# Performance work log

Measured on AMD Instinct MI355X. Metric: run time of the kernel, lower is better.

Reference implementation:

```python
import jax, jax.numpy as jnp
import numpy as np

K, D, B, T = 512, 256, 32, 4096

def setup_inputs() -> dict:
    key = jax.random.key(0)
    k1, k2 = jax.random.split(key)
    z_e_x = jax.random.normal(k1, (B, D, T), dtype=jnp.float32)
    # nn.Embedding weight init uniform(-1/K, 1/K)
    emb_weight = jax.random.uniform(k2, (K, D), dtype=jnp.float32, minval=-1.0 / K, maxval=1.0 / K)
    return {"z_e_x": z_e_x, "emb_weight": emb_weight}

def reference(z_e_x, emb_weight):
    # forward(): permute [B,D,T] -> [B,T,D], nearest-codebook indices
    z = jnp.transpose(z_e_x, (0, 2, 1))  # [B, T, D]
    # squared L2 distances: ||z||^2 - 2 z.W^T + ||W||^2  -> [B, T, K]
    z_sq = jnp.sum(z * z, axis=-1, keepdims=True)           # [B, T, 1]
    w_sq = jnp.sum(emb_weight * emb_weight, axis=-1)        # [K]
    cross = jnp.einsum('btd,kd->btk', z, emb_weight)        # [B, T, K]
    dists = z_sq - 2.0 * cross + w_sq[None, None, :]
    latents = jnp.argmin(dists, axis=-1)                    # [B, T] int
    return latents
```

## Files before the change

kernel.cpp:

```cpp
#include <hip/hip_runtime.h>
#include <math.h>

#define NK 512
#define DD 256
#define NB 32
#define NT 4096

typedef __attribute__((ext_vector_type(8))) _Float16 f16x8;
typedef __attribute__((ext_vector_type(4))) float f32x4;

#define MARGIN 1.5e-4f
#define DCH 16
#define NCH 16
#define APAD 40

__device__ __forceinline__ unsigned short f16bits(float x) {
    _Float16 h = (_Float16)x;
    unsigned short s;
    __builtin_memcpy(&s, &h, 2);
    return s;
}

__global__ __launch_bounds__(512) void prep_kernel(const float* __restrict__ W,
                                                   unsigned short* __restrict__ Wpp,
                                                   float* __restrict__ wsq,
                                                   int* __restrict__ gcnt) {
    const int bx = blockIdx.x;
    const int k  = threadIdx.x;
    if (bx < NCH) {
        const int d0 = bx * DCH;
        float w[16];
        const float4* src4 = (const float4*)(W + (size_t)k * DD + d0);
        #pragma unroll
        for (int q = 0; q < 4; ++q) {
            float4 v = src4[q];
            w[4 * q + 0] = v.x; w[4 * q + 1] = v.y; w[4 * q + 2] = v.z; w[4 * q + 3] = v.w;
        }
        __align__(16) unsigned int dw[16];
        #pragma unroll
        for (int j = 0; j < 16; ++j) {
            unsigned short s = f16bits(w[j] * 4096.0f);
            dw[j] = (unsigned int)s | ((unsigned int)s << 16);
        }
        unsigned short* dst = Wpp + ((size_t)bx * 512 + k) * 32;
        #pragma unroll
        for (int j = 0; j < 4; ++j) ((int4*)dst)[j] = ((const int4*)dw)[j];
    } else {
        const float4* row = (const float4*)(W + (size_t)k * DD);
        double s = 0.0;
        #pragma unroll 8
        for (int i = 0; i < DD / 4; ++i) {
            float4 v = row[i];
            s += (double)v.x * v.x + (double)v.y * v.y + (double)v.z * v.z + (double)v.w * v.w;
        }
        wsq[k] = (float)s;
        if (k == 0) *gcnt = 0;
    }
}

__global__ __launch_bounds__(512, 2) void vq_phase1(const float* __restrict__ Z,
                                                    const unsigned short* __restrict__ Wpp,
                                                    const float* __restrict__ wsq,
                                                    int* __restrict__ out,
                                                    int* __restrict__ gties,
                                                    int* __restrict__ gcnt) {
    __shared__ __align__(16) short As[2][128 * APAD];
    __shared__ __align__(16) short Bs[2][512 * APAD];
    __shared__ double zred[512];
    __shared__ float  zf[128];
    __shared__ float  cb1[512], cb2[512];
    __shared__ int    cbi[512];
    __shared__ int    llist[128];
    __shared__ int    lcnt, gbase;

    const int tid  = threadIdx.x;
    const int wave = tid >> 6;
    const int lane = tid & 63;
    const int lm   = lane & 15;
    const int lq   = lane >> 4;
    const int mw   = wave & 1;
    const int nw   = wave >> 1;

    const int bx = blockIdx.x;
    const int b  = bx >> 5;
    const int t0 = (bx & 31) * 128;

    const int t_l = tid & 127;
    const int dg  = tid >> 7;

    const float* zcol = Z + (size_t)b * DD * NT + t0 + t_l;
    const unsigned short* wrow = Wpp + (size_t)tid * 32;

    if (tid == 0) lcnt = 0;

    f32x4 acc[4][8];
    #pragma unroll
    for (int mt = 0; mt < 4; ++mt)
        #pragma unroll
        for (int nt = 0; nt < 8; ++nt)
            acc[mt][nt] = (f32x4){0.f, 0.f, 0.f, 0.f};

    double zacc = 0.0;

    {
        float zv[4];
        #pragma unroll
        for (int j = 0; j < 4; ++j)
            zv[j] = zcol[(size_t)(dg * 4 + j) * NT];
        int4 wv[4];
        const int4* ws4 = (const int4*)wrow;
        #pragma unroll
        for (int q = 0; q < 4; ++q) wv[q] = ws4[q];

        #pragma unroll
        for (int j = 0; j < 4; ++j) zacc = fma((double)zv[j], (double)zv[j], zacc);
        __align__(16) unsigned int u[4];
        #pragma unroll
        for (int j = 0; j < 4; ++j) {
            _Float16 zh = (_Float16)zv[j];
            float rz = zv[j] - (float)zh;
            unsigned short hs, ls;
            __builtin_memcpy(&hs, &zh, 2);
            ls = f16bits(rz);
            u[j] = (unsigned int)hs | ((unsigned int)ls << 16);
        }
        *(int4*)&As[0][t_l * APAD + dg * 8] = *(const int4*)u;
        int4* bd = (int4*)&Bs[0][tid * APAD];
        bd[0] = wv[0]; bd[1] = wv[1]; bd[2] = wv[2]; bd[3] = wv[3];
    }
    __syncthreads();

    for (int c = 0; c < NCH; ++c) {
        const int cur = c & 1;

        float zv2[4]; int4 wv2[4];
        if (c < NCH - 1) {
            const int d0 = (c + 1) * DCH;
            #pragma unroll
            for (int j = 0; j < 4; ++j)
                zv2[j] = zcol[(size_t)(d0 + dg * 4 + j) * NT];
            const int4* ws4 = (const int4*)(wrow + (size_t)(c + 1) * NK * 32);
            #pragma unroll
            for (int q = 0; q < 4; ++q) wv2[q] = ws4[q];
        }

        f16x8 a[4], bb[8];
        #pragma unroll
        for (int mt = 0; mt < 4; ++mt)
            a[mt] = *(const f16x8*)&As[cur][(mw * 64 + mt * 16 + lm) * APAD + lq * 8];
        #pragma unroll
        for (int nt = 0; nt < 8; ++nt)
            bb[nt] = *(const f16x8*)&Bs[cur][(nw * 128 + nt * 16 + lm) * APAD + lq * 8];
        #pragma unroll
        for (int mt = 0; mt < 4; ++mt)
            #pragma unroll
            for (int nt = 0; nt < 8; ++nt)
                acc[mt][nt] = __builtin_amdgcn_mfma_f32_16x16x32_f16(
                    a[mt], bb[nt], acc[mt][nt], 0, 0, 0);

        if (c < NCH - 1) {
            #pragma unroll
            for (int j = 0; j < 4; ++j) zacc = fma((double)zv2[j], (double)zv2[j], zacc);
            __align__(16) unsigned int u[4];
            #pragma unroll
            for (int j = 0; j < 4; ++j) {
                _Float16 zh = (_Float16)zv2[j];
                float rz = zv2[j] - (float)zh;
                unsigned short hs, ls;
                __builtin_memcpy(&hs, &zh, 2);
                ls = f16bits(rz);
                u[j] = (unsigned int)hs | ((unsigned int)ls << 16);
            }
            *(int4*)&As[cur ^ 1][t_l * APAD + dg * 8] = *(const int4*)u;
            int4* bd = (int4*)&Bs[cur ^ 1][tid * APAD];
            bd[0] = wv2[0]; bd[1] = wv2[1]; bd[2] = wv2[2]; bd[3] = wv2[3];
            __syncthreads();
        }
    }

    zred[dg * 128 + t_l] = zacc;
    __syncthreads();
    if (tid < 128)
        zf[tid] = (float)(((zred[tid] + zred[128 + tid]) + zred[256 + tid]) + zred[384 + tid]);
    __syncthreads();

    float wq[8];
    #pragma unroll
    for (int nt = 0; nt < 8; ++nt)
        wq[nt] = wsq[nw * 128 + nt * 16 + lm];
    const int kbase = nw * 128 + lm;

    #pragma unroll
    for (int mt = 0; mt < 4; ++mt) {
        #pragma unroll
        for (int r = 0; r < 4; ++r) {
            float zz = zf[mw * 64 + mt * 16 + lq * 4 + r];
            float q1 = INFINITY, q2 = INFINITY;
            int i1 = 0x7fffffff;
            #pragma unroll
            for (int nt = 0; nt < 8; ++nt) {
                float c2   = __fmul_rn(acc[mt][nt][r], 4.8828125e-4f);
                float dist = __fadd_rn(__fsub_rn(zz, c2), wq[nt]);
                int kk = kbase + nt * 16;
                if (dist < q1 || (dist == q1 && kk < i1)) { q2 = q1; q1 = dist; i1 = kk; }
                else if (dist < q2) q2 = dist;
            }
            #pragma unroll
            for (int mk = 1; mk <= 8; mk <<= 1) {
                float o1 = __shfl_xor(q1, mk);
                float o2 = __shfl_xor(q2, mk);
                int   oi = __shfl_xor(i1, mk);
                if (o1 < q1 || (o1 == q1 && oi < i1)) { q2 = fminf(q1, o2); q1 = o1; i1 = oi; }
                else { q2 = fminf(o1, q2); }
            }
            if (lm == 0) {
                int m = mw * 64 + mt * 16 + lq * 4 + r;
                cb1[m * 4 + nw] = q1;
                cb2[m * 4 + nw] = q2;
                cbi[m * 4 + nw] = i1;
            }
        }
    }
    __syncthreads();
    if (tid < 128) {
        float q1 = cb1[tid * 4], q2 = cb2[tid * 4];
        int   i1 = cbi[tid * 4];
        #pragma unroll
        for (int p = 1; p < 4; ++p) {
            float c1 = cb1[tid * 4 + p], c2v = cb2[tid * 4 + p];
            int   ci = cbi[tid * 4 + p];
            if (c1 < q1 || (c1 == q1 && ci < i1)) { q2 = fminf(q1, c2v); q1 = c1; i1 = ci; }
            else { q2 = fminf(q2, c1); }
        }
        out[(size_t)b * NT + t0 + tid] = i1;
        if (q2 - q1 <= MARGIN) {
            int p = atomicAdd(&lcnt, 1);
            llist[p] = b * NT + t0 + tid;
        }
    }
    __syncthreads();
    if (tid == 0) gbase = (lcnt > 0) ? atomicAdd(gcnt, lcnt) : 0;
    __syncthreads();
    if (tid < lcnt) gties[gbase + tid] = llist[tid];
}

__global__ __launch_bounds__(256) void vq_fix(const float* __restrict__ Z,
                                              const float* __restrict__ W,
                                              const float* __restrict__ wsq,
                                              const int* __restrict__ gties,
                                              const int* __restrict__ gcnt,
                                              int* __restrict__ out) {
    __shared__ __align__(16) float Zs[8][256];
    __shared__ double pz[8][32];
    __shared__ float  zsqs[8];
    __shared__ int    bts[8];
    __shared__ float  rv[8][4];
    __shared__ int    ri[8][4];

    const int tid  = threadIdx.x;
    const int lane = tid & 63;
    const int wvx  = tid >> 6;
    const int n    = *gcnt;

    for (int base = blockIdx.x * 8; base < n; base += (int)gridDim.x * 8) {
        const int m = (n - base < 8) ? (n - base) : 8;
        __syncthreads();
        if (tid < 8) bts[tid] = gties[base + ((tid < m) ? tid : 0)];
        __syncthreads();

        #pragma unroll
        for (int i = 0; i < 8; ++i) {
            if (i < m) {
                int tb = bts[i];
                int bb = tb >> 12, t = tb & 4095;
                Zs[i][tid] = Z[(size_t)bb * DD * NT + (size_t)tid * NT + t];
            }
        }
        __syncthreads();

        {
            int i = tid >> 5, seg = tid & 31;
            double s = 0.0;
            #pragma unroll
            for (int j = 0; j < 8; ++j) {
                double zz = (double)Zs[i][seg * 8 + j];
                s = fma(zz, zz, s);
            }
            pz[i][seg] = s;
        }
        __syncthreads();
        if (tid < 8) {
            double s = 0.0;
            #pragma unroll
            for (int j = 0; j < 32; ++j) s += pz[tid][j];
            zsqs[tid] = (float)s;
        }
        __syncthreads();

        float da[2][8];
        #pragma unroll
        for (int rr = 0; rr < 2; ++rr) {
            int k = tid + rr * 256;
            const float4* wr = (const float4*)(W + (size_t)k * DD);
            float a8[8];
            #pragma unroll
            for (int i = 0; i < 8; ++i) a8[i] = 0.f;
            #pragma unroll 2
            for (int q = 0; q < 64; ++q) {
                float4 w4 = wr[q];
                #pragma unroll
                for (int i = 0; i < 8; ++i) {
                    float4 z4 = *(const float4*)&Zs[i][4 * q];
                    a8[i] = fmaf(z4.x, w4.x, a8[i]);
                    a8[i] = fmaf(z4.y, w4.y, a8[i]);
                    a8[i] = fmaf(z4.z, w4.z, a8[i]);
                    a8[i] = fmaf(z4.w, w4.w, a8[i]);
                }
            }
            float wqv = wsq[k];
            #pragma unroll
            for (int i = 0; i < 8; ++i)
                da[rr][i] = __fadd_rn(__fsub_rn(zsqs[i], __fmul_rn(2.0f, a8[i])), wqv);
        }

        #pragma unroll
        for (int i = 0; i < 8; ++i) {
            float v = da[0][i]; int ix = tid;
            if (da[1][i] < v) { v = da[1][i]; ix = tid + 256; }
            #pragma unroll
            for (int mk = 1; mk <= 32; mk <<= 1) {
                float ov = __shfl_xor(v, mk);
                int   oi = __shfl_xor(ix, mk);
                if (ov < v || (ov == v && oi < ix)) { v = ov; ix = oi; }
            }
            if (lane == 0) { rv[i][wvx] = v; ri[i][wvx] = ix; }
        }
        __syncthreads();
        if (tid < 8 && tid < m) {
            float v = INFINITY; int ix = 0x7fffffff;
            #pragma unroll
            for (int w = 0; w < 4; ++w) {
                if (rv[tid][w] < v || (rv[tid][w] == v && ri[tid][w] < ix)) {
                    v = rv[tid][w]; ix = ri[tid][w];
                }
            }
            out[bts[tid]] = ix;
        }
    }
}

#define BT 128
#define BK 128
#define DCHUNK 32
#define NKC (NK / BK)
#define NDC (DD / DCHUNK)
#define WSTR (BK + 4)

__global__ __launch_bounds__(256) void vq_fallback(const float* __restrict__ Z,
                                                   const float* __restrict__ W,
                                                   int* __restrict__ out) {
    __shared__ __align__(16) float Zs[DCHUNK * BT];
    __shared__ __align__(16) float Ws[DCHUNK * WSTR];
    __shared__ float wsqs[NK];

    const int tid = threadIdx.x;
    const int tx  = tid & 15;
    const int ty  = tid >> 4;
    const int b   = blockIdx.y;
    const int t0  = blockIdx.x * BT;

    for (int k = tid; k < NK; k += 256) {
        const float4* row = (const float4*)(W + (size_t)k * DD);
        double s = 0.0;
        for (int i = 0; i < DD / 4; ++i) {
            float4 v = row[i];
            s += (double)v.x * v.x + (double)v.y * v.y + (double)v.z * v.z + (double)v.w * v.w;
        }
        wsqs[k] = (float)s;
    }

    const float* Zb = Z + (size_t)b * DD * NT + t0;

    float best[8]; int bidx[8];
    #pragma unroll
    for (int a = 0; a < 8; ++a) { best[a] = INFINITY; bidx[a] = 0x7fffffff; }
    double zsqd[8];
    #pragma unroll
    for (int a = 0; a < 8; ++a) zsqd[a] = 0.0;
    float zsqf[8];

    for (int kc = 0; kc < NKC; ++kc) {
        float acc[8][8];
        #pragma unroll
        for (int a = 0; a < 8; ++a)
            #pragma unroll
            for (int c = 0; c < 8; ++c) acc[a][c] = 0.f;

        for (int dc = 0; dc < NDC; ++dc) {
            const int d0 = dc * DCHUNK;
            __syncthreads();
            #pragma unroll
            for (int i = 0; i < 4; ++i) {
                int f  = tid + i * 256;
                int r  = f >> 5;
                int c4 = f & 31;
                float4 v = *(const float4*)(Zb + (size_t)(d0 + r) * NT + c4 * 4);
                *(float4*)(&Zs[r * BT + c4 * 4]) = v;
            }
            #pragma unroll
            for (int i = 0; i < 4; ++i) {
                int u  = tid + i * 256;
                int k  = u >> 3;
                int rg = u & 7;
                float4 v = *(const float4*)(W + (size_t)(kc * BK + k) * DD + d0 + rg * 4);
                Ws[(rg * 4 + 0) * WSTR + k] = v.x;
                Ws[(rg * 4 + 1) * WSTR + k] = v.y;
                Ws[(rg * 4 + 2) * WSTR + k] = v.z;
                Ws[(rg * 4 + 3) * WSTR + k] = v.w;
            }
            __syncthreads();
            #pragma unroll 4
            for (int d = 0; d < DCHUNK; ++d) {
                float4 z0 = *(const float4*)(&Zs[d * BT + ty * 8]);
                float4 z1 = *(const float4*)(&Zs[d * BT + ty * 8 + 4]);
                float4 w0 = *(const float4*)(&Ws[d * WSTR + tx * 8]);
                float4 w1 = *(const float4*)(&Ws[d * WSTR + tx * 8 + 4]);
                float za[8] = {z0.x, z0.y, z0.z, z0.w, z1.x, z1.y, z1.z, z1.w};
                float wa[8] = {w0.x, w0.y, w0.z, w0.w, w1.x, w1.y, w1.z, w1.w};
                if (kc == 0) {
                    #pragma unroll
                    for (int a = 0; a < 8; ++a)
                        zsqd[a] = fma((double)za[a], (double)za[a], zsqd[a]);
                }
                #pragma unroll
                for (int a = 0; a < 8; ++a)
                    #pragma unroll
                    for (int c = 0; c < 8; ++c)
                        acc[a][c] = fmaf(za[a], wa[c], acc[a][c]);
            }
        }
        if (kc == 0) {
            #pragma unroll
            for (int a = 0; a < 8; ++a) zsqf[a] = (float)zsqd[a];
        }
        #pragma unroll
        for (int c = 0; c < 8; ++c) {
            int   kg = kc * BK + tx * 8 + c;
            float wqv = wsqs[kg];
            #pragma unroll
            for (int a = 0; a < 8; ++a) {
                float c2   = __fmul_rn(2.0f, acc[a][c]);
                float s    = __fsub_rn(zsqf[a], c2);
                float dist = __fadd_rn(s, wqv);
                if (dist < best[a] || (dist == best[a] && kg < bidx[a])) {
                    best[a] = dist; bidx[a] = kg;
                }
            }
        }
    }
    __syncthreads();
    float* redv = Zs;
    int*   redi = (int*)Ws;
    #pragma unroll
    for (int a = 0; a < 8; ++a) {
        int tl2 = ty * 8 + a;
        redv[tl2 * 16 + tx] = best[a];
        redi[tl2 * 16 + tx] = bidx[a];
    }
    __syncthreads();
    if (tid < BT) {
        float bv = INFINITY; int bi = 0x7fffffff;
        #pragma unroll
        for (int j = 0; j < 16; ++j) {
            float v = redv[tid * 16 + j];
            int   i = redi[tid * 16 + j];
            if (v < bv || (v == bv && i < bi)) { bv = v; bi = i; }
        }
        out[(size_t)b * NT + t0 + tid] = bi;
    }
}

extern "C" void kernel_launch(void* const* d_in, const int* in_sizes, int n_in,
                              void* d_out, int out_size, void* d_ws, size_t ws_size,
                              hipStream_t stream) {
    const float* Z = (const float*)d_in[0];
    const float* W = (const float*)d_in[1];
    int* out = (int*)d_out;

    const size_t OFF_WSQ = 0;
    const size_t OFF_CNT = 2048;
    const size_t OFF_WPP = 4096;
    const size_t OFF_TIE = OFF_WPP + 524288;
    const size_t NEED    = OFF_TIE + 524288;

    if (ws_size >= NEED) {
        float* wsq = (float*)((char*)d_ws + OFF_WSQ);
        int*   gcnt = (int*)((char*)d_ws + OFF_CNT);
        unsigned short* wpp = (unsigned short*)((char*)d_ws + OFF_WPP);
        int*   gties = (int*)((char*)d_ws + OFF_TIE);

        prep_kernel<<<dim3(NCH + 1), dim3(512), 0, stream>>>(W, wpp, wsq, gcnt);
        vq_phase1<<<dim3(1024), dim3(512), 0, stream>>>(Z, wpp, wsq, out, gties, gcnt);
        vq_fix<<<dim3(256), dim3(256), 0, stream>>>(Z, W, wsq, gties, gcnt, out);
    } else {
        vq_fallback<<<dim3(NT / BT, NB), dim3(256), 0, stream>>>(Z, W, out);
    }
}
```

Measured before the change: 374.7 us.

## Preload full Z tile in LDS and stream codebook from global into registers

The main kernel now uses 64-token blocks of 256 threads. Each block converts its whole 64x256 Z tile to split fp16 in LDS once, rather than double-buffering 16-wide D chunks with a barrier per chunk. The codebook B fragments are read directly from global/L2 into registers with a one-chunk register prefetch, which removes the LDS staging of W and the per-chunk syncs. The cost is twice as many blocks, each re-reading the full codebook from L2, and higher register pressure from the prefetch buffers. The scratch arrays for the reduction now alias the same LDS buffer.

```diff
diff --git a/kernel.cpp b/kernel.cpp
--- a/kernel.cpp
+++ b/kernel.cpp
@@ -12,7 +12,7 @@
 #define MARGIN 1.5e-4f
 #define DCH 16
 #define NCH 16
-#define APAD 40
+#define ASTR 536
 
 __device__ __forceinline__ unsigned short f16bits(float x) {
     _Float16 h = (_Float16)x;
@@ -58,130 +58,113 @@
     }
 }
 
-__global__ __launch_bounds__(512, 2) void vq_phase1(const float* __restrict__ Z,
+__global__ __launch_bounds__(256, 2) void vq_phase1(const float* __restrict__ Z,
                                                     const unsigned short* __restrict__ Wpp,
                                                     const float* __restrict__ wsq,
                                                     int* __restrict__ out,
                                                     int* __restrict__ gties,
                                                     int* __restrict__ gcnt) {
-    __shared__ __align__(16) short As[2][128 * APAD];
-    __shared__ __align__(16) short Bs[2][512 * APAD];
-    __shared__ double zred[512];
-    __shared__ float  zf[128];
-    __shared__ float  cb1[512], cb2[512];
-    __shared__ int    cbi[512];
-    __shared__ int    llist[128];
-    __shared__ int    lcnt, gbase;
+    __shared__ __align__(16) short As[64 * ASTR];
+    __shared__ int lcnt, gbase;
 
     const int tid  = threadIdx.x;
     const int wave = tid >> 6;
     const int lane = tid & 63;
     const int lm   = lane & 15;
     const int lq   = lane >> 4;
-    const int mw   = wave & 1;
-    const int nw   = wave >> 1;
+    const int nw   = wave;
 
     const int bx = blockIdx.x;
-    const int b  = bx >> 5;
-    const int t0 = (bx & 31) * 128;
-
-    const int t_l = tid & 127;
-    const int dg  = tid >> 7;
+    const int b  = bx >> 6;
+    const int t0 = (bx & 63) * 64;
+
+    const int t_l = tid & 63;
+    const int dgs = tid >> 6;
 
     const float* zcol = Z + (size_t)b * DD * NT + t0 + t_l;
-    const unsigned short* wrow = Wpp + (size_t)tid * 32;
 
     if (tid == 0) lcnt = 0;
 
-    f32x4 acc[4][8];
-    #pragma unroll
-    for (int mt = 0; mt < 4; ++mt)
-        #pragma unroll
-        for (int nt = 0; nt < 8; ++nt)
-            acc[mt][nt] = (f32x4){0.f, 0.f, 0.f, 0.f};
-
     double zacc = 0.0;
-
-    {
-        float zv[4];
-        #pragma unroll
-        for (int j = 0; j < 4; ++j)
-            zv[j] = zcol[(size_t)(dg * 4 + j) * NT];
-        int4 wv[4];
-        const int4* ws4 = (const int4*)wrow;
-        #pragma unroll
-        for (int q = 0; q < 4; ++q) wv[q] = ws4[q];
-
-        #pragma unroll
-        for (int j = 0; j < 4; ++j) zacc = fma((double)zv[j], (double)zv[j], zacc);
-        __align__(16) unsigned int u[4];
-        #pragma unroll
-        for (int j = 0; j < 4; ++j) {
-            _Float16 zh = (_Float16)zv[j];
-            float rz = zv[j] - (float)zh;
-            unsigned short hs, ls;
-            __builtin_memcpy(&hs, &zh, 2);
-            ls = f16bits(rz);
-            u[j] = (unsigned int)hs | ((unsigned int)ls << 16);
-        }
-        *(int4*)&As[0][t_l * APAD + dg * 8] = *(const int4*)u;
-        int4* bd = (int4*)&Bs[0][tid * APAD];
-        bd[0] = wv[0]; bd[1] = wv[1]; bd[2] = wv[2]; bd[3] = wv[3];
-    }
-    __syncthreads();
-
-    for (int c = 0; c < NCH; ++c) {
-        const int cur = c & 1;
-
-        float zv2[4]; int4 wv2[4];
-        if (c < NCH - 1) {
-            const int d0 = (c + 1) * DCH;
-            #pragma unroll
-            for (int j = 0; j < 4; ++j)
-                zv2[j] = zcol[(size_t)(d0 + dg * 4 + j) * NT];
-            const int4* ws4 = (const int4*)(wrow + (size_t)(c + 1) * NK * 32);
-            #pragma unroll
-            for (int q = 0; q < 4; ++q) wv2[q] = ws4[q];
-        }
-
-        f16x8 a[4], bb[8];
-        #pragma unroll
-        for (int mt = 0; mt < 4; ++mt)
-            a[mt] = *(const f16x8*)&As[cur][(mw * 64 + mt * 16 + lm) * APAD + lq * 8];
-        #pragma unroll
-        for (int nt = 0; nt < 8; ++nt)
-            bb[nt] = *(const f16x8*)&Bs[cur][(nw * 128 + nt * 16 + lm) * APAD + lq * 8];
-        #pragma unroll
-        for (int mt = 0; mt < 4; ++mt)
-            #pragma unroll
-            for (int nt = 0; nt < 8; ++nt)
-                acc[mt][nt] = __builtin_amdgcn_mfma_f32_16x16x32_f16(
-                    a[mt], bb[nt], acc[mt][nt], 0, 0, 0);
-
-        if (c < NCH - 1) {
-            #pragma unroll
-            for (int j = 0; j < 4; ++j) zacc = fma((double)zv2[j], (double)zv2[j], zacc);
+    #pragma unroll
+    for (int half = 0; half < 2; ++half) {
+        float zv[32];
+        #pragma unroll
+        for (int j = 0; j < 32; ++j)
+            zv[j] = zcol[(size_t)(dgs * 64 + half * 32 + j) * NT];
+        #pragma unroll
+        for (int j = 0; j < 32; ++j)
+            zacc = fma((double)zv[j], (double)zv[j], zacc);
+        #pragma unroll
+        for (int j0 = 0; j0 < 32; j0 += 4) {
             __align__(16) unsigned int u[4];
             #pragma unroll
-            for (int j = 0; j < 4; ++j) {
-                _Float16 zh = (_Float16)zv2[j];
-                float rz = zv2[j] - (float)zh;
+            for (int q = 0; q < 4; ++q) {
+                float z = zv[j0 + q];
+                _Float16 zh = (_Float16)z;
+                float rz = z - (float)zh;
                 unsigned short hs, ls;
                 __builtin_memcpy(&hs, &zh, 2);
                 ls = f16bits(rz);
-                u[j] = (unsigned int)hs | ((unsigned int)ls << 16);
-            }
-            *(int4*)&As[cur ^ 1][t_l * APAD + dg * 8] = *(const int4*)u;
-            int4* bd = (int4*)&Bs[cur ^ 1][tid * APAD];
-            bd[0] = wv2[0]; bd[1] = wv2[1]; bd[2] = wv2[2]; bd[3] = wv2[3];
-            __syncthreads();
-        }
-    }
-
-    zred[dg * 128 + t_l] = zacc;
-    __syncthreads();
-    if (tid < 128)
-        zf[tid] = (float)(((zred[tid] + zred[128 + tid]) + zred[256 + tid]) + zred[384 + tid]);
+                u[q] = (unsigned int)hs | ((unsigned int)ls << 16);
+            }
+            *(int4*)&As[t_l * ASTR + (dgs * 64 + half * 32 + j0) * 2] = *(const int4*)u;
+        }
+    }
+    __syncthreads();
+
+    const unsigned short* wb = Wpp + ((size_t)(nw * 128 + lm) * 32) + lq * 8;
+
+    f32x4 acc[4][8];
+    #pragma unroll
+    for (int mt = 0; mt < 4; ++mt)
+        #pragma unroll
+        for (int nt = 0; nt < 8; ++nt)
+            acc[mt][nt] = (f32x4){0.f, 0.f, 0.f, 0.f};
+
+    int4 bv0[8], bv1[8];
+    #pragma unroll
+    for (int nt = 0; nt < 8; ++nt)
+        bv0[nt] = *(const int4*)(wb + nt * 512);
+
+    #pragma unroll
+    for (int c = 0; c < NCH; ++c) {
+        int4* cur = (c & 1) ? bv1 : bv0;
+        int4* nxt = (c & 1) ? bv0 : bv1;
+        if (c < NCH - 1) {
+            const unsigned short* wp = wb + (size_t)(c + 1) * 16384;
+            #pragma unroll
+            for (int nt = 0; nt < 8; ++nt)
+                nxt[nt] = *(const int4*)(wp + nt * 512);
+        }
+        f16x8 a[4];
+        #pragma unroll
+        for (int mt = 0; mt < 4; ++mt)
+            a[mt] = *(const f16x8*)&As[(mt * 16 + lm) * ASTR + c * 32 + lq * 8];
+        #pragma unroll
+        for (int mt = 0; mt < 4; ++mt)
+            #pragma unroll
+            for (int nt = 0; nt < 8; ++nt)
+                acc[mt][nt] = __builtin_amdgcn_mfma_f32_16x16x32_f16(
+                    a[mt], *(const f16x8*)&cur[nt], acc[mt][nt], 0, 0, 0);
+    }
+
+    __syncthreads();
+    double* zred = (double*)As;
+    float*  zf   = (float*)(As + 1024);
+    float*  cb1  = (float*)(As + 1536);
+    float*  cb2  = (float*)(As + 2048);
+    int*    cbi  = (int*)(As + 2560);
+    int*    llist = (int*)(As + 3072);
+
+    zred[dgs * 64 + t_l] = zacc;
+    __syncthreads();
+    if (tid < 64) {
+        double s = zred[tid];
+        #pragma unroll
+        for (int p = 1; p < 4; ++p) s += zred[p * 64 + tid];
+        zf[tid] = (float)s;
+    }
     __syncthreads();
 
     float wq[8];
@@ -194,7 +177,7 @@
     for (int mt = 0; mt < 4; ++mt) {
         #pragma unroll
         for (int r = 0; r < 4; ++r) {
-            float zz = zf[mw * 64 + mt * 16 + lq * 4 + r];
+            float zz = zf[mt * 16 + lq * 4 + r];
             float q1 = INFINITY, q2 = INFINITY;
             int i1 = 0x7fffffff;
             #pragma unroll
@@ -214,7 +197,7 @@
                 else { q2 = fminf(o1, q2); }
             }
             if (lm == 0) {
-                int m = mw * 64 + mt * 16 + lq * 4 + r;
+                int m = mt * 16 + lq * 4 + r;
                 cb1[m * 4 + nw] = q1;
                 cb2[m * 4 + nw] = q2;
                 cbi[m * 4 + nw] = i1;
@@ -222,7 +205,7 @@
         }
     }
     __syncthreads();
-    if (tid < 128) {
+    if (tid < 64) {
         float q1 = cb1[tid * 4], q2 = cb2[tid * 4];
         int   i1 = cbi[tid * 4];
         #pragma unroll
@@ -500,7 +483,7 @@
         int*   gties = (int*)((char*)d_ws + OFF_TIE);
 
         prep_kernel<<<dim3(NCH + 1), dim3(512), 0, stream>>>(W, wpp, wsq, gcnt);
-        vq_phase1<<<dim3(1024), dim3(512), 0, stream>>>(Z, wpp, wsq, out, gties, gcnt);
+        vq_phase1<<<dim3(2048), dim3(256), 0, stream>>>(Z, wpp, wsq, out, gties, gcnt);
         vq_fix<<<dim3(256), dim3(256), 0, stream>>>(Z, W, wsq, gties, gcnt, out);
     } else {
         vq_fallback<<<dim3(NT / BT, NB), dim3(256), 0, stream>>>(Z, W, out);
```

Result: faster. 340.3 us (-9.2%).
